# Performance work log

Measured on AMD Instinct MI355X. Metric: run time of the kernel, lower is better.

The kernel has to match this reference:

```python
import jax, jax.numpy as jnp
import numpy as np

EPS = 1e-3  # freq_scaling_eps default

def _mean_transf(mu, sigma, w, p):
    return jnp.exp(-0.5 * (sigma * w) ** 2) * jnp.sin(p + mu * w)

def _var_transf(mu, sigma, w, p):
    return 0.5 - 0.5 * jnp.exp(-2 * (sigma * w) ** 2) * jnp.cos(2 * (p + mu * w)) - _mean_transf(mu, sigma, w, p) ** 2

def setup_inputs() -> dict:
    key = jax.random.key(0)
    k1, k2, k3, k4 = jax.random.split(key, 4)
    B, IN, F, OUT = 8192, 512, 64, 512
    x = jax.random.normal(k1, (B, IN), dtype=jnp.float32)
    freqs = jax.random.normal(k2, (1, 1, F), dtype=jnp.float32)  # normal(stddev=1.0) init
    phases = jnp.zeros((1, 1, F), dtype=jnp.float32)             # zeros init
    # variance_scaling(1.0,'fan_in',uniform): limit = sqrt(3/fan_in)
    lim_b = np.sqrt(3.0 / F)
    beta = jax.random.uniform(k3, (F, OUT), dtype=jnp.float32, minval=-lim_b, maxval=lim_b)
    lim_l = np.sqrt(3.0 / IN)
    lamb = jax.random.uniform(k4, (IN, OUT), dtype=jnp.float32, minval=-lim_l, maxval=lim_l)
    bias = jnp.zeros((OUT,), dtype=jnp.float32)
    return {"x": x, "freqs": freqs, "phases": phases, "beta": beta, "lamb": lamb, "bias": bias}

def reference(x, freqs, phases, beta, lamb, bias):
    # x: [B, I]; freqs/phases: [1, 1, F]; beta: [F, O]; lamb: [I, O]; bias: [O]
    xb = jnp.sin(freqs * x[:, :, None] + phases)  # [B, I, F]
    mean = _mean_transf(0.0, 1.0, freqs, phases)  # [1, 1, F]
    var = _var_transf(0.0, 1.0, freqs, phases)    # [1, 1, F]
    xb = (xb - mean) / jnp.sqrt(EPS + var)
    out = jnp.einsum('bif,fo,io->bo', xb, beta, lamb)  # bilinear contraction
    return out + bias
```

## Files before the change

### kernel.cpp

```cpp
#include <hip/hip_runtime.h>
#include <hip/hip_bf16.h>


#define TB 256

typedef __attribute__((ext_vector_type(8))) short short8;
typedef __attribute__((ext_vector_type(4))) float floatx4;
typedef __attribute__((ext_vector_type(4))) unsigned int uintx4;
typedef __attribute__((ext_vector_type(8))) unsigned short ushort8t;

__device__ __forceinline__ unsigned pk_bf16(float a, float b) {
    union { float f; unsigned u; } ca, cb;
    ca.f = a; cb.f = b;
    unsigned ua = ca.u + 0x8000u;
    unsigned ub = cb.u + 0x8000u;
    return __builtin_amdgcn_perm(ub, ua, 0x07060302u);
}
__device__ __forceinline__ unsigned short f_to_bf16u(float v) {
    union { __hip_bfloat16 h; unsigned short u; } cv;
    cv.h = __float2bfloat16(v);
    return cv.u;
}
__device__ __forceinline__ float bf16u_to_f(unsigned short v) {
    union { unsigned u; float f; } cv; cv.u = ((unsigned)v) << 16; return cv.f;
}

__device__ __forceinline__ uintx4 sin_pack8(const float xv[8], float wfr, float pfr) {
    float s[8];
    #pragma unroll
    for (int j = 0; j < 8; ++j) {
        float t = fmaf(xv[j], wfr, pfr);
        float u = t - __builtin_rintf(t);
        s[j] = __builtin_amdgcn_sinf(u);
    }
    uintx4 w4;
    w4.x = pk_bf16(s[0], s[1]); w4.y = pk_bf16(s[2], s[3]);
    w4.z = pk_bf16(s[4], s[5]); w4.w = pk_bf16(s[6], s[7]);
    return w4;
}

__global__ __launch_bounds__(TB, 2)
void actlayer_kernel(const float* __restrict__ x,
                     const float* __restrict__ freqs,
                     const float* __restrict__ phases,
                     const float* __restrict__ beta,
                     const float* __restrict__ lamb,
                     const float* __restrict__ bias,
                     float* __restrict__ out)
{
    constexpr int I = 512, F = 64, O = 512;
    const int t  = threadIdx.x;
    const int bx = blockIdx.x;
    const int bn = bx & 1;
    const int bm = bx >> 1;
    const int n0 = bn * 256;
    const int m0 = bm * 32;

    __shared__ __align__(16) unsigned short A_sh[2][2][32][72];
    __shared__ __align__(16) unsigned short L_scr[128][72];
    __shared__ __align__(16) unsigned short brP_sh[F][16][16];
    __shared__ float wrev_sh[F], prev_sh[F], r_sh[F], m_sh[F];
    __shared__ float c_sh[256];

    if (t < F) {
        float wq = freqs[t];
        float ph = phases[t];
        float e1 = expf(-0.5f * wq * wq);
        float mean = e1 * sinf(ph);
        float e2 = expf(-2.0f * wq * wq);
        float var = 0.5f - 0.5f * e2 * cosf(2.0f * ph) - mean * mean;
        float r = 1.0f / sqrtf(1e-3f + var);
        wrev_sh[t] = wq * 0.15915494309189535f;
        prev_sh[t] = ph * 0.15915494309189535f;
        r_sh[t] = r;
        m_sh[t] = mean;
    }
    __syncthreads();
    #pragma unroll
    for (int j = 0; j < 64; ++j) {
        int e = t + TB * j;
        int f = e >> 8;
        int rem = e & 255;
        int w = rem >> 4;
        int c = rem & 15;
        float bv = beta[f * O + n0 + w * 16 + c] * r_sh[f];
        brP_sh[f][c][w] = f_to_bf16u(bv);
    }
    __syncthreads();
    {
        int c = t & 15, w = t >> 4;
        float sb = 0.f;
        #pragma unroll
        for (int f = 0; f < F; ++f) sb += bf16u_to_f(brP_sh[f][c][w]) * m_sh[f];
        float sl = 0.f;
        const float* lp = lamb + n0 + t;
        #pragma unroll 8
        for (int i = 0; i < I; ++i) sl += lp[(size_t)i * O];
        c_sh[t] = bias[n0 + t] - sb * sl;
    }

    const int lane = t & 63;
    const int wid  = t >> 6;
    const int mg   = wid >> 1;
    const int ng   = wid & 1;
    const int l15  = lane & 15;
    const int quad = lane >> 4;
    const int kr = t & 7;
    const int r0 = t >> 3;
    const int nL  = t & 127;
    const int khL = t >> 7;

    floatx4 oacc[8];
    #pragma unroll
    for (int nt = 0; nt < 8; ++nt) oacc[nt] = (floatx4){0.f, 0.f, 0.f, 0.f};
    const floatx4 zero4 = (floatx4){0.f, 0.f, 0.f, 0.f};

    #pragma unroll 1
    for (int it = 0; it < 8; ++it) {
        const int i0 = it * 64;
        {
            const float* lp = lamb + (size_t)(i0 + khL * 32) * O + n0 + nL;
            float v[32];
            #pragma unroll
            for (int k = 0; k < 32; ++k) v[k] = lp[(size_t)k * O];
            #pragma unroll
            for (int rr = 0; rr < 4; ++rr) {
                uintx4 w4;
                w4.x = pk_bf16(v[rr*8+0], v[rr*8+1]);
                w4.y = pk_bf16(v[rr*8+2], v[rr*8+3]);
                w4.z = pk_bf16(v[rr*8+4], v[rr*8+5]);
                w4.w = pk_bf16(v[rr*8+6], v[rr*8+7]);
                *(uintx4*)&L_scr[nL][khL * 32 + rr * 8] = w4;
            }
        }
        float xs[8];
        {
            const float* xp = x + (size_t)(m0 + r0) * I + i0 + kr * 8;
            float4 a0 = *(const float4*)(xp);
            float4 a1 = *(const float4*)(xp + 4);
            xs[0]=a0.x; xs[1]=a0.y; xs[2]=a0.z; xs[3]=a0.w;
            xs[4]=a1.x; xs[5]=a1.y; xs[6]=a1.z; xs[7]=a1.w;
        }
        __syncthreads();
        short8 lf[2][8];
        if (ng == 0) {
            #pragma unroll
            for (int kk = 0; kk < 2; ++kk)
                #pragma unroll
                for (int nt = 0; nt < 8; ++nt)
                    lf[kk][nt] = *(const short8*)&L_scr[nt*16 + l15][kk*32 + quad*8];
        }
        __syncthreads();
        {
            const float* lp = lamb + (size_t)(i0 + khL * 32) * O + n0 + 128 + nL;
            float v[32];
            #pragma unroll
            for (int k = 0; k < 32; ++k) v[k] = lp[(size_t)k * O];
            #pragma unroll
            for (int rr = 0; rr < 4; ++rr) {
                uintx4 w4;
                w4.x = pk_bf16(v[rr*8+0], v[rr*8+1]);
                w4.y = pk_bf16(v[rr*8+2], v[rr*8+3]);
                w4.z = pk_bf16(v[rr*8+4], v[rr*8+5]);
                w4.w = pk_bf16(v[rr*8+6], v[rr*8+7]);
                *(uintx4*)&L_scr[nL][khL * 32 + rr * 8] = w4;
            }
        }
        *(uintx4*)&A_sh[0][0][r0][kr * 8] = sin_pack8(xs, wrev_sh[0], prev_sh[0]);
        *(uintx4*)&A_sh[0][1][r0][kr * 8] = sin_pack8(xs, wrev_sh[1], prev_sh[1]);
        __syncthreads();
        if (ng == 1) {
            #pragma unroll
            for (int kk = 0; kk < 2; ++kk)
                #pragma unroll
                for (int nt = 0; nt < 8; ++nt)
                    lf[kk][nt] = *(const short8*)&L_scr[nt*16 + l15][kk*32 + quad*8];
        }

        int cur = 0;
        #pragma unroll 1
        for (int f = 0; f < F; f += 2) {
            ushort8t bruA = *(const ushort8t*)&brP_sh[f][l15][ng * 8];
            ushort8t bruB = *(const ushort8t*)&brP_sh[f + 1][l15][ng * 8];
            const int arow = mg * 16 + l15;
            short8 afA0 = *(const short8*)&A_sh[cur][0][arow][quad * 8];
            short8 afA1 = *(const short8*)&A_sh[cur][0][arow][32 + quad * 8];
            short8 afB0 = *(const short8*)&A_sh[cur][1][arow][quad * 8];
            short8 afB1 = *(const short8*)&A_sh[cur][1][arow][32 + quad * 8];
            float brA[8], brB[8];
            #pragma unroll
            for (int q = 0; q < 8; ++q) {
                brA[q] = bf16u_to_f(bruA[q]);
                brB[q] = bf16u_to_f(bruB[q]);
            }
            const bool more = (f + 2 < F);
            if (more) {
                *(uintx4*)&A_sh[cur ^ 1][0][r0][kr * 8] =
                    sin_pack8(xs, wrev_sh[f + 2], prev_sh[f + 2]);
            }
            #pragma unroll
            for (int nt = 0; nt < 8; ++nt) {
                floatx4 s = __builtin_amdgcn_mfma_f32_16x16x32_bf16(
                    afA0, lf[0][nt], zero4, 0, 0, 0);
                s = __builtin_amdgcn_mfma_f32_16x16x32_bf16(
                    afA1, lf[1][nt], s, 0, 0, 0);
                oacc[nt] += brA[nt] * s;
            }
            if (more) {
                *(uintx4*)&A_sh[cur ^ 1][1][r0][kr * 8] =
                    sin_pack8(xs, wrev_sh[f + 3], prev_sh[f + 3]);
            }
            #pragma unroll
            for (int nt = 0; nt < 8; ++nt) {
                floatx4 s = __builtin_amdgcn_mfma_f32_16x16x32_bf16(
                    afB0, lf[0][nt], zero4, 0, 0, 0);
                s = __builtin_amdgcn_mfma_f32_16x16x32_bf16(
                    afB1, lf[1][nt], s, 0, 0, 0);
                oacc[nt] += brB[nt] * s;
            }
            __syncthreads();
            cur ^= 1;
        }
    }

    #pragma unroll
    for (int nt = 0; nt < 8; ++nt) {
        int gn = n0 + ng * 128 + nt * 16 + l15;
        float cv = c_sh[ng * 128 + nt * 16 + l15];
        int gm = m0 + mg * 16 + quad * 4;
        #pragma unroll
        for (int rg = 0; rg < 4; ++rg) {
            out[(size_t)(gm + rg) * O + gn] = oacc[nt][rg] + cv;
        }
    }
}

extern "C" void kernel_launch(void* const* d_in, const int* in_sizes, int n_in,
                              void* d_out, int out_size, void* d_ws, size_t ws_size,
                              hipStream_t stream) {
    const float* x      = (const float*)d_in[0];
    const float* freqs  = (const float*)d_in[1];
    const float* phases = (const float*)d_in[2];
    const float* beta   = (const float*)d_in[3];
    const float* lamb   = (const float*)d_in[4];
    const float* bias   = (const float*)d_in[5];
    float* out = (float*)d_out;

    dim3 grid(512);
    dim3 block(TB);
    hipLaunchKernelGGL(actlayer_kernel, grid, block, 0, stream,
                       x, freqs, phases, beta, lamb, bias, out);
}
```

Before: 404.3 us.

## Tile blocks over full output width to stop duplicating sine feature work

Blocks now cover 16 rows by all 512 output columns, with each of the four waves owning 128 columns, instead of 32 rows by 256 columns split over two N-halves. Before, the sin basis for each row was computed twice, once per column half; now it is computed once, halving the transcendental work. Each block also stages and converts the full lambda slice, so lambda reads and bf16 packing per block double. The bf16 beta*r table in LDS is dropped. Beta is now read from global memory inside the f loop and scaled by r in fp32, which adds memory loads to the hot loop.

```diff
diff --git a/kernel.cpp b/kernel.cpp
--- a/kernel.cpp
+++ b/kernel.cpp
@@ -6,8 +6,8 @@
 
 typedef __attribute__((ext_vector_type(8))) short short8;
 typedef __attribute__((ext_vector_type(4))) float floatx4;
+typedef __attribute__((ext_vector_type(2))) unsigned int uintx2;
 typedef __attribute__((ext_vector_type(4))) unsigned int uintx4;
-typedef __attribute__((ext_vector_type(8))) unsigned short ushort8t;
 
 __device__ __forceinline__ unsigned pk_bf16(float a, float b) {
     union { float f; unsigned u; } ca, cb;
@@ -16,27 +16,19 @@
     unsigned ub = cb.u + 0x8000u;
     return __builtin_amdgcn_perm(ub, ua, 0x07060302u);
 }
-__device__ __forceinline__ unsigned short f_to_bf16u(float v) {
-    union { __hip_bfloat16 h; unsigned short u; } cv;
-    cv.h = __float2bfloat16(v);
-    return cv.u;
-}
-__device__ __forceinline__ float bf16u_to_f(unsigned short v) {
-    union { unsigned u; float f; } cv; cv.u = ((unsigned)v) << 16; return cv.f;
-}
-
-__device__ __forceinline__ uintx4 sin_pack8(const float xv[8], float wfr, float pfr) {
-    float s[8];
-    #pragma unroll
-    for (int j = 0; j < 8; ++j) {
-        float t = fmaf(xv[j], wfr, pfr);
-        float u = t - __builtin_rintf(t);
+
+__device__ __forceinline__ uintx2 sin_pack4(const float xv[4], float wfr, float pfr) {
+    float s[4];
+    #pragma unroll
+    for (int j = 0; j < 4; ++j) {
+        float tt = fmaf(xv[j], wfr, pfr);
+        float u = tt - __builtin_rintf(tt);
         s[j] = __builtin_amdgcn_sinf(u);
     }
-    uintx4 w4;
-    w4.x = pk_bf16(s[0], s[1]); w4.y = pk_bf16(s[2], s[3]);
-    w4.z = pk_bf16(s[4], s[5]); w4.w = pk_bf16(s[6], s[7]);
-    return w4;
+    uintx2 r;
+    r.x = pk_bf16(s[0], s[1]);
+    r.y = pk_bf16(s[2], s[3]);
+    return r;
 }
 
 __global__ __launch_bounds__(TB, 2)
@@ -50,17 +42,12 @@
 {
     constexpr int I = 512, F = 64, O = 512;
     const int t  = threadIdx.x;
-    const int bx = blockIdx.x;
-    const int bn = bx & 1;
-    const int bm = bx >> 1;
-    const int n0 = bn * 256;
-    const int m0 = bm * 32;
-
-    __shared__ __align__(16) unsigned short A_sh[2][2][32][72];
-    __shared__ __align__(16) unsigned short L_scr[128][72];
-    __shared__ __align__(16) unsigned short brP_sh[F][16][16];
+    const int m0 = blockIdx.x * 16;
+
+    __shared__ __align__(16) unsigned short A_sh[2][2][16][72];
+    __shared__ __align__(16) unsigned short L_sh[256][72];
     __shared__ float wrev_sh[F], prev_sh[F], r_sh[F], m_sh[F];
-    __shared__ float c_sh[256];
+    __shared__ float c_sh[512];
 
     if (t < F) {
         float wq = freqs[t];
@@ -77,126 +64,124 @@
     }
     __syncthreads();
     #pragma unroll
-    for (int j = 0; j < 64; ++j) {
-        int e = t + TB * j;
-        int f = e >> 8;
-        int rem = e & 255;
-        int w = rem >> 4;
-        int c = rem & 15;
-        float bv = beta[f * O + n0 + w * 16 + c] * r_sh[f];
-        brP_sh[f][c][w] = f_to_bf16u(bv);
-    }
-    __syncthreads();
-    {
-        int c = t & 15, w = t >> 4;
+    for (int j = 0; j < 2; ++j) {
+        int col = t + 256 * j;
         float sb = 0.f;
-        #pragma unroll
-        for (int f = 0; f < F; ++f) sb += bf16u_to_f(brP_sh[f][c][w]) * m_sh[f];
+        #pragma unroll 8
+        for (int f = 0; f < F; ++f) sb += beta[f * O + col] * (r_sh[f] * m_sh[f]);
         float sl = 0.f;
-        const float* lp = lamb + n0 + t;
         #pragma unroll 8
-        for (int i = 0; i < I; ++i) sl += lp[(size_t)i * O];
-        c_sh[t] = bias[n0 + t] - sb * sl;
+        for (int i = 0; i < I; ++i) sl += lamb[(size_t)i * O + col];
+        c_sh[col] = bias[col] - sb * sl;
     }
 
     const int lane = t & 63;
-    const int wid  = t >> 6;
-    const int mg   = wid >> 1;
-    const int ng   = wid & 1;
+    const int ng   = t >> 6;
     const int l15  = lane & 15;
     const int quad = lane >> 4;
-    const int kr = t & 7;
-    const int r0 = t >> 3;
-    const int nL  = t & 127;
-    const int khL = t >> 7;
+    const int r0s  = t >> 4;
+    const int kqs  = t & 15;
 
     floatx4 oacc[8];
     #pragma unroll
     for (int nt = 0; nt < 8; ++nt) oacc[nt] = (floatx4){0.f, 0.f, 0.f, 0.f};
     const floatx4 zero4 = (floatx4){0.f, 0.f, 0.f, 0.f};
+
+    const float* bp = beta + ng * 128 + l15;
 
     #pragma unroll 1
     for (int it = 0; it < 8; ++it) {
         const int i0 = it * 64;
+        float xs[4];
         {
-            const float* lp = lamb + (size_t)(i0 + khL * 32) * O + n0 + nL;
-            float v[32];
-            #pragma unroll
-            for (int k = 0; k < 32; ++k) v[k] = lp[(size_t)k * O];
-            #pragma unroll
-            for (int rr = 0; rr < 4; ++rr) {
-                uintx4 w4;
-                w4.x = pk_bf16(v[rr*8+0], v[rr*8+1]);
-                w4.y = pk_bf16(v[rr*8+2], v[rr*8+3]);
-                w4.z = pk_bf16(v[rr*8+4], v[rr*8+5]);
-                w4.w = pk_bf16(v[rr*8+6], v[rr*8+7]);
-                *(uintx4*)&L_scr[nL][khL * 32 + rr * 8] = w4;
-            }
-        }
-        float xs[8];
+            float4 xv = *(const float4*)(x + (size_t)(m0 + r0s) * I + i0 + kqs * 4);
+            xs[0] = xv.x; xs[1] = xv.y; xs[2] = xv.z; xs[3] = xv.w;
+        }
         {
-            const float* xp = x + (size_t)(m0 + r0) * I + i0 + kr * 8;
-            float4 a0 = *(const float4*)(xp);
-            float4 a1 = *(const float4*)(xp + 4);
-            xs[0]=a0.x; xs[1]=a0.y; xs[2]=a0.z; xs[3]=a0.w;
-            xs[4]=a1.x; xs[5]=a1.y; xs[6]=a1.z; xs[7]=a1.w;
-        }
+            const float* lp = lamb + (size_t)i0 * O + t;
+            #pragma unroll
+            for (int h = 0; h < 2; ++h) {
+                float v[32];
+                #pragma unroll
+                for (int k = 0; k < 32; ++k) v[k] = lp[(size_t)(h * 32 + k) * O];
+                #pragma unroll
+                for (int rr = 0; rr < 4; ++rr) {
+                    uintx4 w4;
+                    w4.x = pk_bf16(v[rr*8+0], v[rr*8+1]);
+                    w4.y = pk_bf16(v[rr*8+2], v[rr*8+3]);
+                    w4.z = pk_bf16(v[rr*8+4], v[rr*8+5]);
+                    w4.w = pk_bf16(v[rr*8+6], v[rr*8+7]);
+                    *(uintx4*)&L_sh[t][h * 32 + rr * 8] = w4;
+                }
+            }
+        }
+        *(uintx2*)&A_sh[0][0][r0s][kqs * 4] = sin_pack4(xs, wrev_sh[0], prev_sh[0]);
+        *(uintx2*)&A_sh[0][1][r0s][kqs * 4] = sin_pack4(xs, wrev_sh[1], prev_sh[1]);
         __syncthreads();
         short8 lf[2][8];
-        if (ng == 0) {
+        if (ng < 2) {
             #pragma unroll
             for (int kk = 0; kk < 2; ++kk)
                 #pragma unroll
                 for (int nt = 0; nt < 8; ++nt)
-                    lf[kk][nt] = *(const short8*)&L_scr[nt*16 + l15][kk*32 + quad*8];
+                    lf[kk][nt] = *(const short8*)&L_sh[ng*128 + nt*16 + l15][kk*32 + quad*8];
         }
         __syncthreads();
         {
-            const float* lp = lamb + (size_t)(i0 + khL * 32) * O + n0 + 128 + nL;
-            float v[32];
-            #pragma unroll
-            for (int k = 0; k < 32; ++k) v[k] = lp[(size_t)k * O];
-            #pragma unroll
-            for (int rr = 0; rr < 4; ++rr) {
-                uintx4 w4;
-                w4.x = pk_bf16(v[rr*8+0], v[rr*8+1]);
-                w4.y = pk_bf16(v[rr*8+2], v[rr*8+3]);
-                w4.z = pk_bf16(v[rr*8+4], v[rr*8+5]);
-                w4.w = pk_bf16(v[rr*8+6], v[rr*8+7]);
-                *(uintx4*)&L_scr[nL][khL * 32 + rr * 8] = w4;
-            }
-        }
-        *(uintx4*)&A_sh[0][0][r0][kr * 8] = sin_pack8(xs, wrev_sh[0], prev_sh[0]);
-        *(uintx4*)&A_sh[0][1][r0][kr * 8] = sin_pack8(xs, wrev_sh[1], prev_sh[1]);
+            const float* lp = lamb + (size_t)i0 * O + 256 + t;
+            #pragma unroll
+            for (int h = 0; h < 2; ++h) {
+                float v[32];
+                #pragma unroll
+                for (int k = 0; k < 32; ++k) v[k] = lp[(size_t)(h * 32 + k) * O];
+                #pragma unroll
+                for (int rr = 0; rr < 4; ++rr) {
+                    uintx4 w4;
+                    w4.x = pk_bf16(v[rr*8+0], v[rr*8+1]);
+                    w4.y = pk_bf16(v[rr*8+2], v[rr*8+3]);
+                    w4.z = pk_bf16(v[rr*8+4], v[rr*8+5]);
+                    w4.w = pk_bf16(v[rr*8+6], v[rr*8+7]);
+                    *(uintx4*)&L_sh[t][h * 32 + rr * 8] = w4;
+                }
+            }
+        }
         __syncthreads();
-        if (ng == 1) {
+        if (ng >= 2) {
             #pragma unroll
             for (int kk = 0; kk < 2; ++kk)
                 #pragma unroll
                 for (int nt = 0; nt < 8; ++nt)
-                    lf[kk][nt] = *(const short8*)&L_scr[nt*16 + l15][kk*32 + quad*8];
-        }
+                    lf[kk][nt] = *(const short8*)&L_sh[(ng-2)*128 + nt*16 + l15][kk*32 + quad*8];
+        }
+
+        float bA[8], bB[8];
+        #pragma unroll
+        for (int nt = 0; nt < 8; ++nt) {
+            bA[nt] = bp[0 * O + nt * 16];
+            bB[nt] = bp[1 * O + nt * 16];
+        }
+        float rA = r_sh[0], rB = r_sh[1];
 
         int cur = 0;
         #pragma unroll 1
         for (int f = 0; f < F; f += 2) {
-            ushort8t bruA = *(const ushort8t*)&brP_sh[f][l15][ng * 8];
-            ushort8t bruB = *(const ushort8t*)&brP_sh[f + 1][l15][ng * 8];
-            const int arow = mg * 16 + l15;
-            short8 afA0 = *(const short8*)&A_sh[cur][0][arow][quad * 8];
-            short8 afA1 = *(const short8*)&A_sh[cur][0][arow][32 + quad * 8];
-            short8 afB0 = *(const short8*)&A_sh[cur][1][arow][quad * 8];
-            short8 afB1 = *(const short8*)&A_sh[cur][1][arow][32 + quad * 8];
+            short8 afA0 = *(const short8*)&A_sh[cur][0][l15][quad * 8];
+            short8 afA1 = *(const short8*)&A_sh[cur][0][l15][32 + quad * 8];
+            short8 afB0 = *(const short8*)&A_sh[cur][1][l15][quad * 8];
+            short8 afB1 = *(const short8*)&A_sh[cur][1][l15][32 + quad * 8];
             float brA[8], brB[8];
             #pragma unroll
-            for (int q = 0; q < 8; ++q) {
-                brA[q] = bf16u_to_f(bruA[q]);
-                brB[q] = bf16u_to_f(bruB[q]);
-            }
+            for (int q = 0; q < 8; ++q) { brA[q] = bA[q] * rA; brB[q] = bB[q] * rB; }
             const bool more = (f + 2 < F);
             if (more) {
-                *(uintx4*)&A_sh[cur ^ 1][0][r0][kr * 8] =
-                    sin_pack8(xs, wrev_sh[f + 2], prev_sh[f + 2]);
+                #pragma unroll
+                for (int nt = 0; nt < 8; ++nt) {
+                    bA[nt] = bp[(f + 2) * O + nt * 16];
+                    bB[nt] = bp[(f + 3) * O + nt * 16];
+                }
+                rA = r_sh[f + 2]; rB = r_sh[f + 3];
+                *(uintx2*)&A_sh[cur ^ 1][0][r0s][kqs * 4] =
+                    sin_pack4(xs, wrev_sh[f + 2], prev_sh[f + 2]);
             }
             #pragma unroll
             for (int nt = 0; nt < 8; ++nt) {
@@ -207,8 +192,8 @@
                 oacc[nt] += brA[nt] * s;
             }
             if (more) {
-                *(uintx4*)&A_sh[cur ^ 1][1][r0][kr * 8] =
-                    sin_pack8(xs, wrev_sh[f + 3], prev_sh[f + 3]);
+                *(uintx2*)&A_sh[cur ^ 1][1][r0s][kqs * 4] =
+                    sin_pack4(xs, wrev_sh[f + 3], prev_sh[f + 3]);
             }
             #pragma unroll
             for (int nt = 0; nt < 8; ++nt) {
@@ -225,9 +210,9 @@
 
     #pragma unroll
     for (int nt = 0; nt < 8; ++nt) {
-        int gn = n0 + ng * 128 + nt * 16 + l15;
-        float cv = c_sh[ng * 128 + nt * 16 + l15];
-        int gm = m0 + mg * 16 + quad * 4;
+        int gn = ng * 128 + nt * 16 + l15;
+        float cv = c_sh[gn];
+        int gm = m0 + quad * 4;
         #pragma unroll
         for (int rg = 0; rg < 4; ++rg) {
             out[(size_t)(gm + rg) * O + gn] = oacc[nt][rg] + cv;
```

New measurement: 419.0 us. 1.04x slower.
